# Optimization experiments

Hardware: AMD Instinct MI355X
Metric: run time of the kernel (lower is better)

The kernel has to match this reference:

```python
import jax, jax.numpy as jnp
import numpy as np

HEADS = 8
DIM_HEAD = 64
QUERY_DIM = 512
CONTEXT_DIM = 512
OUT_DIM = 512
INNER = HEADS * DIM_HEAD  # 512


def setup_inputs() -> dict:
    key = jax.random.key(0)
    ks = jax.random.split(key, 6)
    B, N, S, M = 2, 1024, 4, 2048
    x = jax.random.normal(ks[0], (B, N, S, QUERY_DIM), dtype=jnp.float32)
    context = jax.random.normal(ks[1], (B, M, CONTEXT_DIM), dtype=jnp.float32)
    # Linear weights stored as [in, out] so y = x @ W (matches torch Linear with W.T)
    Wq = jax.random.normal(ks[2], (QUERY_DIM, INNER), dtype=jnp.float32) / np.sqrt(QUERY_DIM)
    Wkv = jax.random.normal(ks[3], (CONTEXT_DIM, 2 * INNER), dtype=jnp.float32) / np.sqrt(CONTEXT_DIM)
    Wo = jax.random.normal(ks[4], (INNER, OUT_DIM), dtype=jnp.float32) / np.sqrt(INNER)
    bo = jax.random.normal(ks[5], (OUT_DIM,), dtype=jnp.float32) * 0.01
    return {"x": x, "context": context, "Wq": Wq, "Wkv": Wkv, "Wo": Wo, "bo": bo}


def reference(x, context, Wq, Wkv, Wo, bo):
    B, N, S, _ = x.shape
    M = context.shape[1]
    scale = DIM_HEAD ** -0.5
    # projections
    q = (x @ Wq).reshape(B, N, S, HEADS, DIM_HEAD)            # b n s h d
    kv = context @ Wkv                                        # b m (2*inner)
    k, v = jnp.split(kv, 2, axis=-1)
    k = k.reshape(B, M, HEADS, DIM_HEAD)                      # b m h d
    v = v.reshape(B, M, HEADS, DIM_HEAD)
    # attention scores: [(b h) s n m] expressed as bhsnm
    sim = jnp.einsum('bnshd,bmhd->bhsnm', q, k) * scale
    attn = jax.nn.softmax(sim, axis=-1)
    out = jnp.einsum('bhsnm,bmhd->bnshd', attn, v)            # b n s h d
    out = out.reshape(B, N, S, INNER)
    return out @ Wo + bo
```

## Files before the change

kernel.cpp:

```cpp
#include <hip/hip_runtime.h>

typedef __bf16 bf16;
typedef __bf16 bf16x8 __attribute__((ext_vector_type(8)));
typedef __bf16 bf16x4 __attribute__((ext_vector_type(4)));
typedef float f32x4 __attribute__((ext_vector_type(4)));

#define SCL 0.18033688011112042f

#define GLOAD_LDS16(g, l)                                          \
  __builtin_amdgcn_global_load_lds(                                \
      (const __attribute__((address_space(1))) void*)(g),          \
      (__attribute__((address_space(3))) void*)(l), 16, 0, 0)

__global__ __launch_bounds__(256) void prep_kernel(const float* __restrict__ x,
                                                   const float* __restrict__ ctx,
                                                   const float* __restrict__ Wq,
                                                   const float* __restrict__ Wkv,
                                                   const float* __restrict__ Wo,
                                                   bf16* __restrict__ xb,
                                                   bf16* __restrict__ cb,
                                                   bf16* __restrict__ Wqt,
                                                   bf16* __restrict__ Wkvt,
                                                   bf16* __restrict__ Wot) {
  const int bid = blockIdx.x;
  const int tid = threadIdx.x;
  if (bid < 3072) {
    const float* src;
    bf16* dst;
    size_t off;
    if (bid < 2048) { src = x; dst = xb; off = (size_t)bid * 2048; }
    else            { src = ctx; dst = cb; off = (size_t)(bid - 2048) * 2048; }
    size_t i = off + (size_t)tid * 8;
    float4 a0 = *(const float4*)&src[i];
    float4 a1 = *(const float4*)&src[i + 4];
    bf16x8 o;
    o[0] = (bf16)a0.x; o[1] = (bf16)a0.y; o[2] = (bf16)a0.z; o[3] = (bf16)a0.w;
    o[4] = (bf16)a1.x; o[5] = (bf16)a1.y; o[6] = (bf16)a1.z; o[7] = (bf16)a1.w;
    *(bf16x8*)&dst[i] = o;
  } else {
    __shared__ float tile[32][33];
    const int idx = bid - 3072;
    const int bx = idx & 63;
    const int k0 = (idx >> 6) * 32;
    const float* W; bf16* Wt; int N, n0;
    if (bx < 16)      { W = Wq;  Wt = Wqt;  N = 512;  n0 = bx * 32; }
    else if (bx < 48) { W = Wkv; Wt = Wkvt; N = 1024; n0 = (bx - 16) * 32; }
    else              { W = Wo;  Wt = Wot;  N = 512;  n0 = (bx - 48) * 32; }
    const int j = tid & 31, i0 = tid >> 5;
#pragma unroll
    for (int ii = 0; ii < 4; ii++) {
      int i = i0 * 4 + ii;
      tile[i][j] = W[(size_t)(k0 + i) * N + n0 + j];
    }
    __syncthreads();
#pragma unroll
    for (int ii = 0; ii < 4; ii++) {
      int i = i0 * 4 + ii;
      Wt[(size_t)(n0 + i) * 512 + k0 + j] = (bf16)tile[j][i];
    }
  }
}

__device__ __forceinline__ void gemm128x64_core(const bf16* __restrict__ A,
                                                const bf16* __restrict__ Bt,
                                                int m0, int n0,
                                                bf16* As, bf16* Bs,
                                                f32x4 (&acc)[4][2],
                                                int wave, int lane) {
  const int l15 = lane & 15, quad = lane >> 4;
  const int psw = l15 & 7;
  const int lrow = lane >> 3;
  const int gchunk = (lane & 7) ^ lrow;
  const bf16* Ag = A + (size_t)(m0 + wave * 32 + lrow) * 512 + gchunk * 8;
  const bf16* Bg = Bt + (size_t)(n0 + wave * 16 + lrow) * 512 + gchunk * 8;
  bf16* Asw = As + wave * 32 * 64;
  bf16* Bsw = Bs + wave * 16 * 64;
  const int wm = (wave >> 1) * 64, wn = (wave & 1) * 32;

  for (int kt = 0; kt < 512; kt += 64) {
#pragma unroll
    for (int g = 0; g < 4; g++)
      GLOAD_LDS16(Ag + kt + (size_t)(g * 8) * 512, Asw + g * 8 * 64);
#pragma unroll
    for (int g = 0; g < 2; g++)
      GLOAD_LDS16(Bg + kt + (size_t)(g * 8) * 512, Bsw + g * 8 * 64);
    __syncthreads();
#pragma unroll
    for (int h = 0; h < 2; h++) {
      bf16x8 af[4], bfr[2];
#pragma unroll
      for (int i = 0; i < 4; i++)
        af[i] = *(const bf16x8*)&As[(wm + i * 16 + l15) * 64 + (((h * 4 + quad) ^ psw) * 8)];
#pragma unroll
      for (int j = 0; j < 2; j++)
        bfr[j] = *(const bf16x8*)&Bs[(wn + j * 16 + l15) * 64 + (((h * 4 + quad) ^ psw) * 8)];
#pragma unroll
      for (int i = 0; i < 4; i++)
#pragma unroll
        for (int j = 0; j < 2; j++)
          acc[i][j] = __builtin_amdgcn_mfma_f32_16x16x32_bf16(af[i], bfr[j], acc[i][j], 0, 0, 0);
    }
    __syncthreads();
  }
}

__global__ __launch_bounds__(256, 2) void proj_kernel(const bf16* __restrict__ xb,
                                                      const bf16* __restrict__ cb,
                                                      const bf16* __restrict__ Wqt,
                                                      const bf16* __restrict__ Wkvt,
                                                      bf16* __restrict__ qb,
                                                      bf16* __restrict__ Kb,
                                                      bf16* __restrict__ Vtb) {
  __shared__ __align__(16) bf16 As[128 * 64];
  __shared__ __align__(16) bf16 Bs[64 * 64];
  const int tid = threadIdx.x;
  const int wave = tid >> 6, lane = tid & 63;
  const int quad = lane >> 4, l15 = lane & 15;
  const int bid = blockIdx.x;
  f32x4 acc[4][2] = {};
  const int wm = (wave >> 1) * 64, wn = (wave & 1) * 32;

  if (bid < 512) {
    const int m0 = (bid & 63) * 128, n0 = (bid >> 6) * 64;
    gemm128x64_core(xb, Wqt, m0, n0, As, Bs, acc, wave, lane);
#pragma unroll
    for (int i = 0; i < 4; i++) {
      const int rowb = m0 + wm + i * 16 + quad * 4;
#pragma unroll
      for (int j = 0; j < 2; j++) {
        const int col = n0 + wn + j * 16 + l15;
#pragma unroll
        for (int r = 0; r < 4; r++)
          qb[(size_t)(rowb + r) * 512 + col] = (bf16)(acc[i][j][r] * SCL);
      }
    }
  } else {
    const int idx = bid - 512;
    const int m0 = (idx & 31) * 128, n0 = (idx >> 5) * 64;
    gemm128x64_core(cb, Wkvt, m0, n0, As, Bs, acc, wave, lane);
#pragma unroll
    for (int i = 0; i < 4; i++) {
      const int rowb = m0 + wm + i * 16 + quad * 4;
#pragma unroll
      for (int j = 0; j < 2; j++) {
        const int col = n0 + wn + j * 16 + l15;
        if (col < 512) {
#pragma unroll
          for (int r = 0; r < 4; r++)
            Kb[(size_t)(rowb + r) * 512 + col] = (bf16)acc[i][j][r];
        } else {
          const int hh = (col - 512) >> 6, d = (col - 512) & 63;
          const int bb = rowb >> 11, mb = rowb & 2047;
          bf16x4 pk;
          pk[0] = (bf16)acc[i][j][0]; pk[1] = (bf16)acc[i][j][1];
          pk[2] = (bf16)acc[i][j][2]; pk[3] = (bf16)acc[i][j][3];
          *(bf16x4*)&Vtb[((size_t)(bb * 8 + hh) * 64 + d) * 2048 + mb] = pk;
        }
      }
    }
  }
}

__global__ __launch_bounds__(256, 2) void outproj_kernel(const bf16* __restrict__ attn,
                                                         const bf16* __restrict__ Wot,
                                                         float* __restrict__ out,
                                                         const float* __restrict__ bias) {
  __shared__ __align__(16) bf16 As[128 * 64];
  __shared__ __align__(16) bf16 Bs[64 * 64];
  const int tid = threadIdx.x;
  const int wave = tid >> 6, lane = tid & 63;
  const int quad = lane >> 4, l15 = lane & 15;
  const int bid = blockIdx.x;
  const int m0 = (bid & 63) * 128, n0 = (bid >> 6) * 64;
  f32x4 acc[4][2] = {};
  gemm128x64_core(attn, Wot, m0, n0, As, Bs, acc, wave, lane);
  const int wm = (wave >> 1) * 64, wn = (wave & 1) * 32;
#pragma unroll
  for (int i = 0; i < 4; i++) {
    const int rowb = m0 + wm + i * 16 + quad * 4;
#pragma unroll
    for (int j = 0; j < 2; j++) {
      const int col = n0 + wn + j * 16 + l15;
      const float bv = bias[col];
#pragma unroll
      for (int r = 0; r < 4; r++)
        out[(size_t)(rowb + r) * 512 + col] = acc[i][j][r] + bv;
    }
  }
}

__global__ __launch_bounds__(256, 2) void attn_kernel(const bf16* __restrict__ q,
                                                      const bf16* __restrict__ Kb,
                                                      const bf16* __restrict__ Vtb,
                                                      bf16* __restrict__ attn_out) {
  const int tid = threadIdx.x;
  const int wave = tid >> 6, lane = tid & 63;
  const int quad = lane >> 4, l15 = lane & 15;
  const int bid = blockIdx.x;
  const int g = bid & 15, inner = bid >> 4;
  const int b = g >> 3, h = g & 7;
  const int s = inner & 3, nt = inner >> 2;
  const int n0 = nt * 128;

  __shared__ __align__(16) bf16 Kl[2][64 * 64];
  __shared__ __align__(16) bf16 Vl[2][64 * 64];
  __shared__ __align__(16) bf16 Pl[4][32 * 64];
  bf16* Pw = &Pl[wave][0];

  size_t qoff[2];
  bf16x8 qf[2][2];
#pragma unroll
  for (int cg = 0; cg < 2; cg++) {
    const int n = n0 + wave * 32 + cg * 16 + l15;
    qoff[cg] = ((size_t)((b * 1024 + n) * 4 + s)) * 512 + h * 64;
    qf[cg][0] = *(const bf16x8*)&q[qoff[cg] + quad * 8];
    qf[cg][1] = *(const bf16x8*)&q[qoff[cg] + 32 + quad * 8];
  }

  f32x4 o[2][4] = {};
  f32x4 ol[2] = {};
  bf16x8 ones;
#pragma unroll
  for (int i = 0; i < 8; i++) ones[i] = (bf16)1.0f;

  const int srow = tid >> 2, c0 = tid & 3;
  const bf16* Kg = Kb + (size_t)(b * 2048 + srow) * 512 + h * 64 + c0 * 16;
  const bf16* Vg = Vtb + ((size_t)(b * 8 + h) * 64 + srow) * 2048 + c0 * 16;
  const int ssw = srow & 7;
  const int koff0 = srow * 64 + ((c0 * 2) ^ ssw) * 8;
  const int koff1 = srow * 64 + ((c0 * 2 + 1) ^ ssw) * 8;

  uint4 kr0 = *(const uint4*)Kg;
  uint4 kr1 = *(const uint4*)(Kg + 8);
  uint4 vr0 = *(const uint4*)Vg;
  uint4 vr1 = *(const uint4*)(Vg + 8);
  *(uint4*)&Kl[0][koff0] = kr0; *(uint4*)&Kl[0][koff1] = kr1;
  *(uint4*)&Vl[0][koff0] = vr0; *(uint4*)&Vl[0][koff1] = vr1;

  const int psw = l15 & 7;

  for (int t = 0; t < 32; ++t) {
    __syncthreads();
    if (t < 31) {
      const bf16* kg = Kg + (size_t)(t + 1) * 64 * 512;
      const bf16* vg = Vg + (t + 1) * 64;
      kr0 = *(const uint4*)kg; kr1 = *(const uint4*)(kg + 8);
      vr0 = *(const uint4*)vg; vr1 = *(const uint4*)(vg + 8);
    }
    const bf16* Kc = &Kl[t & 1][0];
    const bf16* Vc = &Vl[t & 1][0];

    f32x4 sf[2][4];
#pragma unroll
    for (int mc = 0; mc < 4; mc++) {
      bf16x8 kf0 = *(const bf16x8*)&Kc[(mc * 16 + l15) * 64 + ((quad ^ psw) * 8)];
      bf16x8 kf1 = *(const bf16x8*)&Kc[(mc * 16 + l15) * 64 + (((4 + quad) ^ psw) * 8)];
#pragma unroll
      for (int cg = 0; cg < 2; cg++) {
        f32x4 z = {};
        z = __builtin_amdgcn_mfma_f32_16x16x32_bf16(kf0, qf[cg][0], z, 0, 0, 0);
        z = __builtin_amdgcn_mfma_f32_16x16x32_bf16(kf1, qf[cg][1], z, 0, 0, 0);
        sf[cg][mc] = z;
      }
    }

#pragma unroll
    for (int cg = 0; cg < 2; cg++)
#pragma unroll
      for (int mc = 0; mc < 4; mc++) {
        bf16x4 pk;
        pk[0] = (bf16)__builtin_amdgcn_exp2f(sf[cg][mc][0]);
        pk[1] = (bf16)__builtin_amdgcn_exp2f(sf[cg][mc][1]);
        pk[2] = (bf16)__builtin_amdgcn_exp2f(sf[cg][mc][2]);
        pk[3] = (bf16)__builtin_amdgcn_exp2f(sf[cg][mc][3]);
        *(bf16x4*)&Pw[(cg * 16 + l15) * 64 + (((mc * 2 + (quad >> 1)) ^ psw)) * 8 + (quad & 1) * 4] = pk;
      }

#pragma unroll
    for (int mch = 0; mch < 2; mch++) {
      bf16x8 pf[2];
#pragma unroll
      for (int cg = 0; cg < 2; cg++)
        pf[cg] = *(const bf16x8*)&Pw[(cg * 16 + l15) * 64 + (((mch * 4 + quad) ^ psw)) * 8];
#pragma unroll
      for (int dg = 0; dg < 4; dg++) {
        bf16x8 vf = *(const bf16x8*)&Vc[(dg * 16 + l15) * 64 + (((mch * 4 + quad) ^ psw)) * 8];
#pragma unroll
        for (int cg = 0; cg < 2; cg++)
          o[cg][dg] = __builtin_amdgcn_mfma_f32_16x16x32_bf16(vf, pf[cg], o[cg][dg], 0, 0, 0);
      }
#pragma unroll
      for (int cg = 0; cg < 2; cg++)
        ol[cg] = __builtin_amdgcn_mfma_f32_16x16x32_bf16(ones, pf[cg], ol[cg], 0, 0, 0);
    }

    if (t < 31) {
      bf16* Kn = &Kl[(t + 1) & 1][0];
      bf16* Vn = &Vl[(t + 1) & 1][0];
      *(uint4*)&Kn[koff0] = kr0; *(uint4*)&Kn[koff1] = kr1;
      *(uint4*)&Vn[koff0] = vr0; *(uint4*)&Vn[koff1] = vr1;
    }
  }

#pragma unroll
  for (int cg = 0; cg < 2; cg++) {
    const float inv = 1.0f / ol[cg][0];
#pragma unroll
    for (int dg = 0; dg < 4; dg++) {
      bf16x4 ok;
      ok[0] = (bf16)(o[cg][dg][0] * inv); ok[1] = (bf16)(o[cg][dg][1] * inv);
      ok[2] = (bf16)(o[cg][dg][2] * inv); ok[3] = (bf16)(o[cg][dg][3] * inv);
      *(bf16x4*)&attn_out[qoff[cg] + dg * 16 + quad * 4] = ok;
    }
  }
}

extern "C" void kernel_launch(void* const* d_in, const int* in_sizes, int n_in,
                              void* d_out, int out_size, void* d_ws, size_t ws_size,
                              hipStream_t stream) {
  const float* x = (const float*)d_in[0];
  const float* context = (const float*)d_in[1];
  const float* Wq = (const float*)d_in[2];
  const float* Wkv = (const float*)d_in[3];
  const float* Wo = (const float*)d_in[4];
  const float* bo = (const float*)d_in[5];
  float* out = (float*)d_out;

  char* ws = (char*)d_ws;
  bf16* xb   = (bf16*)(ws);
  bf16* cb   = (bf16*)(ws + (8u << 20));
  bf16* qb   = (bf16*)(ws + (12u << 20));
  bf16* Kb   = (bf16*)(ws + (20u << 20));
  bf16* Vtb  = (bf16*)(ws + (24u << 20));
  bf16* Wqt  = (bf16*)(ws + (28u << 20));
  bf16* Wkvt = (bf16*)(ws + (28u << 20) + 524288);
  bf16* Wot  = (bf16*)(ws + (28u << 20) + 1572864);
  bf16* attn = xb;

  prep_kernel<<<4096, 256, 0, stream>>>(x, context, Wq, Wkv, Wo, xb, cb, Wqt, Wkvt, Wot);
  proj_kernel<<<1024, 256, 0, stream>>>(xb, cb, Wqt, Wkvt, qb, Kb, Vtb);
  attn_kernel<<<512, 256, 0, stream>>>(qb, Kb, Vtb, attn);
  outproj_kernel<<<512, 256, 0, stream>>>(attn, Wot, out, bo);
}
```

Measured before the change: 155.9 us.

## Double-buffer GEMM LDS tiles and pass attention probabilities via lane permutes

The shared GEMM core now double-buffers the A/B LDS tiles, issuing the next k-tile's global-to-LDS loads before computing the current one. This hides load latency but doubles shared memory per block. The attention kernel no longer round-trips the exponentiated scores through LDS. It packs them to bf16 and rearranges them across lanes with permlane32/16 swaps into MFMA operand layout. It also raises wave priority around the MFMA section. There is only one __syncthreads per GEMM iteration before overwriting the other buffer, so correctness depends on the remaining barrier placement.

Measured after the change: 151.3 us. -2.9%, faster.

```diff
diff --git a/kernel.cpp b/kernel.cpp
--- a/kernel.cpp
+++ b/kernel.cpp
@@ -11,6 +11,20 @@
   __builtin_amdgcn_global_load_lds(                                \
       (const __attribute__((address_space(1))) void*)(g),          \
       (__attribute__((address_space(3))) void*)(l), 16, 0, 0)
+
+static __device__ __forceinline__ unsigned pk_bf16(float a, float b) {
+  union { bf16 h[2]; unsigned u; } cv;
+  cv.h[0] = (bf16)a; cv.h[1] = (bf16)b;
+  return cv.u;
+}
+static __device__ __forceinline__ void pl32swap(unsigned& a, unsigned& b) {
+  auto r = __builtin_amdgcn_permlane32_swap(a, b, false, false);
+  a = r[0]; b = r[1];
+}
+static __device__ __forceinline__ void pl16swap(unsigned& a, unsigned& b) {
+  auto r = __builtin_amdgcn_permlane16_swap(a, b, false, false);
+  a = r[0]; b = r[1];
+}
 
 __global__ __launch_bounds__(256) void prep_kernel(const float* __restrict__ x,
                                                    const float* __restrict__ ctx,
@@ -77,23 +91,36 @@
   bf16* Bsw = Bs + wave * 16 * 64;
   const int wm = (wave >> 1) * 64, wn = (wave & 1) * 32;
 
-  for (int kt = 0; kt < 512; kt += 64) {
-#pragma unroll
-    for (int g = 0; g < 4; g++)
-      GLOAD_LDS16(Ag + kt + (size_t)(g * 8) * 512, Asw + g * 8 * 64);
-#pragma unroll
-    for (int g = 0; g < 2; g++)
-      GLOAD_LDS16(Bg + kt + (size_t)(g * 8) * 512, Bsw + g * 8 * 64);
-    __syncthreads();
+#pragma unroll
+  for (int g = 0; g < 4; g++)
+    GLOAD_LDS16(Ag + (size_t)(g * 8) * 512, Asw + g * 8 * 64);
+#pragma unroll
+  for (int g = 0; g < 2; g++)
+    GLOAD_LDS16(Bg + (size_t)(g * 8) * 512, Bsw + g * 8 * 64);
+  __syncthreads();
+
+  for (int t = 0; t < 8; t++) {
+    if (t < 7) {
+      const int kt = (t + 1) * 64;
+      const int nb = (t + 1) & 1;
+#pragma unroll
+      for (int g = 0; g < 4; g++)
+        GLOAD_LDS16(Ag + kt + (size_t)(g * 8) * 512, Asw + nb * (128 * 64) + g * 8 * 64);
+#pragma unroll
+      for (int g = 0; g < 2; g++)
+        GLOAD_LDS16(Bg + kt + (size_t)(g * 8) * 512, Bsw + nb * (64 * 64) + g * 8 * 64);
+    }
+    const bf16* Ac = As + (t & 1) * (128 * 64);
+    const bf16* Bc = Bs + (t & 1) * (64 * 64);
 #pragma unroll
     for (int h = 0; h < 2; h++) {
       bf16x8 af[4], bfr[2];
 #pragma unroll
       for (int i = 0; i < 4; i++)
-        af[i] = *(const bf16x8*)&As[(wm + i * 16 + l15) * 64 + (((h * 4 + quad) ^ psw) * 8)];
+        af[i] = *(const bf16x8*)&Ac[(wm + i * 16 + l15) * 64 + (((h * 4 + quad) ^ psw) * 8)];
 #pragma unroll
       for (int j = 0; j < 2; j++)
-        bfr[j] = *(const bf16x8*)&Bs[(wn + j * 16 + l15) * 64 + (((h * 4 + quad) ^ psw) * 8)];
+        bfr[j] = *(const bf16x8*)&Bc[(wn + j * 16 + l15) * 64 + (((h * 4 + quad) ^ psw) * 8)];
 #pragma unroll
       for (int i = 0; i < 4; i++)
 #pragma unroll
@@ -111,8 +138,8 @@
                                                       bf16* __restrict__ qb,
                                                       bf16* __restrict__ Kb,
                                                       bf16* __restrict__ Vtb) {
-  __shared__ __align__(16) bf16 As[128 * 64];
-  __shared__ __align__(16) bf16 Bs[64 * 64];
+  __shared__ __align__(16) bf16 As[2 * 128 * 64];
+  __shared__ __align__(16) bf16 Bs[2 * 64 * 64];
   const int tid = threadIdx.x;
   const int wave = tid >> 6, lane = tid & 63;
   const int quad = lane >> 4, l15 = lane & 15;
@@ -165,8 +192,8 @@
                                                          const bf16* __restrict__ Wot,
                                                          float* __restrict__ out,
                                                          const float* __restrict__ bias) {
-  __shared__ __align__(16) bf16 As[128 * 64];
-  __shared__ __align__(16) bf16 Bs[64 * 64];
+  __shared__ __align__(16) bf16 As[2 * 128 * 64];
+  __shared__ __align__(16) bf16 Bs[2 * 64 * 64];
   const int tid = threadIdx.x;
   const int wave = tid >> 6, lane = tid & 63;
   const int quad = lane >> 4, l15 = lane & 15;
@@ -204,8 +231,6 @@
 
   __shared__ __align__(16) bf16 Kl[2][64 * 64];
   __shared__ __align__(16) bf16 Vl[2][64 * 64];
-  __shared__ __align__(16) bf16 Pl[4][32 * 64];
-  bf16* Pw = &Pl[wave][0];
 
   size_t qoff[2];
   bf16x8 qf[2][2];
@@ -250,6 +275,8 @@
     const bf16* Kc = &Kl[t & 1][0];
     const bf16* Vc = &Vl[t & 1][0];
 
+    __builtin_amdgcn_s_setprio(1);
+
     f32x4 sf[2][4];
 #pragma unroll
     for (int mc = 0; mc < 4; mc++) {
@@ -264,35 +291,57 @@
       }
     }
 
+    unsigned w[2][4][2];
 #pragma unroll
     for (int cg = 0; cg < 2; cg++)
 #pragma unroll
       for (int mc = 0; mc < 4; mc++) {
-        bf16x4 pk;
-        pk[0] = (bf16)__builtin_amdgcn_exp2f(sf[cg][mc][0]);
-        pk[1] = (bf16)__builtin_amdgcn_exp2f(sf[cg][mc][1]);
-        pk[2] = (bf16)__builtin_amdgcn_exp2f(sf[cg][mc][2]);
-        pk[3] = (bf16)__builtin_amdgcn_exp2f(sf[cg][mc][3]);
-        *(bf16x4*)&Pw[(cg * 16 + l15) * 64 + (((mc * 2 + (quad >> 1)) ^ psw)) * 8 + (quad & 1) * 4] = pk;
+        const float e0 = __builtin_amdgcn_exp2f(sf[cg][mc][0]);
+        const float e1 = __builtin_amdgcn_exp2f(sf[cg][mc][1]);
+        const float e2 = __builtin_amdgcn_exp2f(sf[cg][mc][2]);
+        const float e3 = __builtin_amdgcn_exp2f(sf[cg][mc][3]);
+        w[cg][mc][0] = pk_bf16(e0, e1);
+        w[cg][mc][1] = pk_bf16(e2, e3);
+      }
+
+    bf16x8 pf[2][2];
+#pragma unroll
+    for (int cg = 0; cg < 2; cg++)
+#pragma unroll
+      for (int mch = 0; mch < 2; mch++) {
+        unsigned tw0, tw1, tw2, tw3;
+        {
+          unsigned a = w[cg][2 * mch][0], bb2 = w[cg][2 * mch + 1][0];
+          pl32swap(a, bb2);
+          pl16swap(a, bb2);
+          tw0 = a; tw2 = bb2;
+        }
+        {
+          unsigned a = w[cg][2 * mch][1], bb2 = w[cg][2 * mch + 1][1];
+          pl32swap(a, bb2);
+          pl16swap(a, bb2);
+          tw1 = a; tw3 = bb2;
+        }
+        union { unsigned u[4]; bf16x8 v; } cv;
+        cv.u[0] = tw0; cv.u[1] = tw1; cv.u[2] = tw2; cv.u[3] = tw3;
+        pf[mch][cg] = cv.v;
       }
 
 #pragma unroll
     for (int mch = 0; mch < 2; mch++) {
-      bf16x8 pf[2];
-#pragma unroll
-      for (int cg = 0; cg < 2; cg++)
-        pf[cg] = *(const bf16x8*)&Pw[(cg * 16 + l15) * 64 + (((mch * 4 + quad) ^ psw)) * 8];
 #pragma unroll
       for (int dg = 0; dg < 4; dg++) {
         bf16x8 vf = *(const bf16x8*)&Vc[(dg * 16 + l15) * 64 + (((mch * 4 + quad) ^ psw)) * 8];
 #pragma unroll
         for (int cg = 0; cg < 2; cg++)
-          o[cg][dg] = __builtin_amdgcn_mfma_f32_16x16x32_bf16(vf, pf[cg], o[cg][dg], 0, 0, 0);
+          o[cg][dg] = __builtin_amdgcn_mfma_f32_16x16x32_bf16(vf, pf[mch][cg], o[cg][dg], 0, 0, 0);
       }
 #pragma unroll
       for (int cg = 0; cg < 2; cg++)
-        ol[cg] = __builtin_amdgcn_mfma_f32_16x16x32_bf16(ones, pf[cg], ol[cg], 0, 0, 0);
-    }
+        ol[cg] = __builtin_amdgcn_mfma_f32_16x16x32_bf16(ones, pf[mch][cg], ol[cg], 0, 0, 0);
+    }
+
+    __builtin_amdgcn_s_setprio(0);
 
     if (t < 31) {
       bf16* Kn = &Kl[(t + 1) & 1][0];
```
